# Optimization experiments

Measured on AMD Instinct MI355X. Metric: run time of the kernel, lower is better.

## Reference

```python
import jax, jax.numpy as jnp
import numpy as np

B, S, N, D = 2048, 8, 32, 64


def setup_inputs() -> dict:
    key = jax.random.key(0)
    ks = jax.random.split(key, 13)
    s1 = 1.0 / np.sqrt(2 * D + 6)
    s2 = 1.0 / np.sqrt(D)
    s3 = 1.0 / np.sqrt(D // 2)
    return {
        "celestial_tensor": jax.random.normal(ks[0], (B, S, N, D), jnp.float32),
        "theta": jax.random.normal(ks[1], (B, N), jnp.float32),
        "phi": jax.random.normal(ks[2], (B, N), jnp.float32),
        "velocity": jax.random.normal(ks[3], (B, N), jnp.float32),
        "radius": jax.random.uniform(ks[4], (B, N), jnp.float32),
        "longitude": jax.random.normal(ks[5], (B, N), jnp.float32),
        "W1": jax.random.uniform(ks[6], (2 * D + 6, D), jnp.float32, -s1, s1),
        "b1": jax.random.uniform(ks[7], (D,), jnp.float32, -s1, s1),
        "W2": jax.random.uniform(ks[8], (D, D // 2), jnp.float32, -s2, s2),
        "b2": jax.random.uniform(ks[9], (D // 2,), jnp.float32, -s2, s2),
        "W3": jax.random.uniform(ks[10], (D // 2, 1), jnp.float32, -s3, s3),
        "b3": jax.random.uniform(ks[11], (1,), jnp.float32, -s3, s3),
        "phase_weights": jnp.ones((6,), jnp.float32),
    }


def _circ(a, b):
    # circular difference wrapped to (-pi, pi]
    d = a - b
    return jnp.arctan2(jnp.sin(d), jnp.cos(d))


def reference(celestial_tensor, theta, phi, velocity, radius, longitude,
              W1, b1, W2, b2, W3, b3, phase_weights):
    Bb, _, Nn, _ = celestial_tensor.shape
    feats = celestial_tensor[:, -1]  # [B, N, D] last timestep
    ii, jj = np.triu_indices(Nn, 1)  # static upper-tri pair indices, P pairs
    fi = feats[:, ii]  # [B, P, D]
    fj = feats[:, jj]
    td = _circ(theta[:, ii], theta[:, jj])
    pd = _circ(phi[:, ii], phi[:, jj])
    vd = velocity[:, ii] - velocity[:, jj]
    rr = radius[:, ii] / (radius[:, jj] + 1e-8)
    ld = _circ(longitude[:, ii], longitude[:, jj])
    pr = jnp.cos(td) * jnp.cos(pd)  # phase_relationship
    scal = jnp.stack([td, pd, vd, rr, ld, pr], axis=-1)  # [B, P, 6]
    x = jnp.concatenate([fi, fj, scal], axis=-1)  # [B, P, 2D+6]
    h = jax.nn.gelu(x @ W1 + b1, approximate=False)
    h = jax.nn.gelu(h @ W2 + b2, approximate=False)
    edge = jax.nn.sigmoid((h @ W3 + b3)[..., 0])  # [B, P]
    pf = jnp.stack([jnp.abs(td), jnp.abs(pd), jnp.abs(vd),
                    jnp.abs(rr - 1.0), jnp.abs(ld), jnp.abs(pr)], axis=-1)
    gate = jax.nn.sigmoid(jnp.sum(pf * phase_weights, axis=-1))
    fe = edge * gate  # [B, P]
    adj = jnp.zeros((Bb, Nn, Nn), dtype=fe.dtype)
    adj = adj.at[:, ii, jj].set(fe).at[:, jj, ii].set(fe)
    return adj
```

## Files before the change

### kernel.cpp

```cpp
#include <hip/hip_runtime.h>
#include <hip/hip_bf16.h>
#include <math.h>

#define SS 8
#define NN 32
#define DD 64
#define NP 496
#define LDA 68

typedef short v8s __attribute__((ext_vector_type(8)));
typedef float v4f __attribute__((ext_vector_type(4)));
typedef float f2  __attribute__((ext_vector_type(2)));

union FragU { uint4 u; v8s s; };
union Q2    { float4 q; f2 h[2]; };

static __device__ __forceinline__ f2 f2m(float a, float b) { f2 r; r.x = a; r.y = b; return r; }
static __device__ __forceinline__ f2 splat2(float s) { f2 r; r.x = s; r.y = s; return r; }
static __device__ __forceinline__ f2 pk_fma(f2 a, f2 b, f2 c) {
#if __has_builtin(__builtin_elementwise_fma)
    return __builtin_elementwise_fma(a, b, c);
#else
    return f2m(fmaf(a.x, b.x, c.x), fmaf(a.y, b.y, c.y));
#endif
}

__device__ __forceinline__ float wrap_pi(float d) {
    return fmaf(-6.28318530717958647692f, rintf(d * 0.15915494309189533577f), d);
}
__device__ __forceinline__ float sigmoid_(float x) {
    return __builtin_amdgcn_rcpf(1.0f + __expf(-x));
}
__device__ __forceinline__ f2 gelu2(f2 x) {
#if __has_builtin(__builtin_elementwise_max)
    f2 ax = __builtin_elementwise_max(x, -x);
#else
    f2 ax = f2m(fabsf(x.x), fabsf(x.y));
#endif
    f2 az = ax * splat2(0.70710678118654752440f);
    f2 d = pk_fma(splat2(0.078108f), az, splat2(0.000972f));
    d = pk_fma(d, az, splat2(0.230389f));
    d = pk_fma(d, az, splat2(0.278393f));
    d = pk_fma(d, az, splat2(1.0f));
    f2 t = f2m(__builtin_amdgcn_rcpf(d.x), __builtin_amdgcn_rcpf(d.y));
    f2 t2 = t * t;
    f2 a = ax * splat2(0.5f);
    f2 base = pk_fma(x, splat2(0.5f), a);
    f2 u = a * t2;
    return pk_fma(-u, t2, base);
}
__device__ __forceinline__ unsigned int pack_bf16_rne(float x0, float x1) {
    union { __hip_bfloat162 h2; unsigned int u; } cv;
    float2 f; f.x = x0; f.y = x1;
    cv.h2 = __float22bfloat162_rn(f);
    return cv.u;
}
__device__ __forceinline__ float row_reduce16(float x) {
    int v;
    v = __builtin_amdgcn_update_dpp(0, __float_as_int(x), 0x128, 0xf, 0xf, false);
    x += __int_as_float(v);
    v = __builtin_amdgcn_update_dpp(0, __float_as_int(x), 0x124, 0xf, 0xf, false);
    x += __int_as_float(v);
    v = __builtin_amdgcn_update_dpp(0, __float_as_int(x), 0x122, 0xf, 0xf, false);
    x += __int_as_float(v);
    v = __builtin_amdgcn_update_dpp(0, __float_as_int(x), 0x121, 0xf, 0xf, false);
    x += __int_as_float(v);
    return x;
}
__device__ __forceinline__ uint4 build_w2_frag(const float* __restrict__ W2,
                                               int kb, int col) {
    uint4 pk;
    pk.x = pack_bf16_rne(W2[(kb + 0) * 32 + col], W2[(kb + 1) * 32 + col]);
    pk.y = pack_bf16_rne(W2[(kb + 2) * 32 + col], W2[(kb + 3) * 32 + col]);
    pk.z = pack_bf16_rne(W2[(kb + 4) * 32 + col], W2[(kb + 5) * 32 + col]);
    pk.w = pack_bf16_rne(W2[(kb + 6) * 32 + col], W2[(kb + 7) * 32 + col]);
    return pk;
}

__global__ __launch_bounds__(256, 2) void edge_kernel(
    const float* __restrict__ cel,
    const float* __restrict__ theta,
    const float* __restrict__ phi,
    const float* __restrict__ vel,
    const float* __restrict__ rad,
    const float* __restrict__ lon,
    const float* __restrict__ W1,
    const float* __restrict__ b1,
    const float* __restrict__ W2,
    const float* __restrict__ b2,
    const float* __restrict__ W3,
    const float* __restrict__ b3,
    const float* __restrict__ pw,
    float* __restrict__ out)
{
    __shared__ __align__(16) float sAi[NN * LDA];
    __shared__ __align__(16) float sBj[NN * LDA];
    __shared__ __align__(16) float sW1s[6 * 64];
    __shared__ float sAdj[1024];
    __shared__ __align__(16) float sScal[NP * 8];
    __shared__ unsigned char sI[NP], sJ[NP];

    const int b = blockIdx.x;
    const int t = threadIdx.x;
    const int ml = t & 15;
    const int ql = (t >> 4) & 3;
    const int wv = t >> 6;
    const int kA = ql * 8;

    FragU f00, f01, f10, f11;
    f00.u = build_w2_frag(W2, 0 * 32 + kA, 0 * 16 + ml);
    f01.u = build_w2_frag(W2, 1 * 32 + kA, 0 * 16 + ml);
    f10.u = build_w2_frag(W2, 0 * 32 + kA, 1 * 16 + ml);
    f11.u = build_w2_frag(W2, 1 * 32 + kA, 1 * 16 + ml);
    const float b2v0 = b2[ml], b2v1 = b2[16 + ml];
    const float w3v0 = W3[ml], w3v1 = W3[16 + ml];
    const float b3s  = b3[0];

    if (t < 31) {
        int off = t * 31 - (t * (t - 1)) / 2;
        for (int j = t + 1; j < 32; ++j) {
            sI[off] = (unsigned char)t;
            sJ[off] = (unsigned char)j;
            ++off;
        }
    }
    for (int idx = t; idx < 1024; idx += 256) sAdj[idx] = 0.0f;
    for (int idx = t; idx < 384; idx += 256) sW1s[idx] = W1[128 * 64 + idx];
    __syncthreads();

    for (int p = t; p < NP; p += 256) {
        const int i = sI[p], j = sJ[p];
        const float td = wrap_pi(theta[b * NN + i] - theta[b * NN + j]);
        const float pd = wrap_pi(phi[b * NN + i] - phi[b * NN + j]);
        const float vd = vel[b * NN + i] - vel[b * NN + j];
        const float rr = rad[b * NN + i] * __builtin_amdgcn_rcpf(rad[b * NN + j] + 1e-8f);
        const float ld = wrap_pi(lon[b * NN + i] - lon[b * NN + j]);
        const float pr = __cosf(td) * __cosf(pd);
        const float pf = fabsf(td) * pw[0] + fabsf(pd) * pw[1]
                       + fabsf(vd) * pw[2] + fabsf(rr - 1.0f) * pw[3]
                       + fabsf(ld) * pw[4] + fabsf(pr) * pw[5];
        const int sw = (p >> 2) & 1;
        float4* c0 = (float4*)&sScal[p * 8 + (sw << 2)];
        float4* c1 = (float4*)&sScal[p * 8 + ((sw ^ 1) << 2)];
        *c0 = float4{td, pd, vd, rr};
        *c1 = float4{ld, pr, sigmoid_(pf), 0.0f};
    }

    {
        const int col = t & 63;
        const int w   = __builtin_amdgcn_readfirstlane(t >> 6);
        const float* fbase = cel + ((size_t)b * SS + (SS - 1)) * (NN * DD);
        f2 accA[8], accB[8];
        #pragma unroll
        for (int m = 0; m < 8; ++m) { accA[m] = splat2(0.0f); accB[m] = splat2(0.0f); }
        for (int k4 = 0; k4 < 64; k4 += 4) {
            const f2 wa01 = f2m(W1[(k4 + 0) * 64 + col], W1[(k4 + 1) * 64 + col]);
            const f2 wa23 = f2m(W1[(k4 + 2) * 64 + col], W1[(k4 + 3) * 64 + col]);
            const f2 wb01 = f2m(W1[(k4 + 64) * 64 + col], W1[(k4 + 65) * 64 + col]);
            const f2 wb23 = f2m(W1[(k4 + 66) * 64 + col], W1[(k4 + 67) * 64 + col]);
            #pragma unroll
            for (int m = 0; m < 8; ++m) {
                const float4 fv = *(const float4*)&fbase[(w + 4 * m) * 64 + k4];
                accA[m] = pk_fma(f2m(fv.x, fv.y), wa01, accA[m]);
                accA[m] = pk_fma(f2m(fv.z, fv.w), wa23, accA[m]);
                accB[m] = pk_fma(f2m(fv.x, fv.y), wb01, accB[m]);
                accB[m] = pk_fma(f2m(fv.z, fv.w), wb23, accB[m]);
            }
        }
        const float b1c = b1[col];
        #pragma unroll
        for (int m = 0; m < 8; ++m) {
            sAi[(w + 4 * m) * LDA + col] = accA[m].x + accA[m].y + b1c;
            sBj[(w + 4 * m) * LDA + col] = accB[m].x + accB[m].y;
        }
    }
    __syncthreads();

    f2 w1f[6][8];
    #pragma unroll
    for (int s = 0; s < 6; ++s) {
        Q2 u0, u1, u2, u3;
        u0.q = *(const float4*)&sW1s[s * 64 + kA];
        u1.q = *(const float4*)&sW1s[s * 64 + kA + 4];
        u2.q = *(const float4*)&sW1s[s * 64 + 32 + kA];
        u3.q = *(const float4*)&sW1s[s * 64 + 36 + kA];
        w1f[s][0] = u0.h[0]; w1f[s][1] = u0.h[1];
        w1f[s][2] = u1.h[0]; w1f[s][3] = u1.h[1];
        w1f[s][4] = u2.h[0]; w1f[s][5] = u2.h[1];
        w1f[s][6] = u3.h[0]; w1f[s][7] = u3.h[1];
    }

    #pragma clang loop unroll(disable)
    for (int r = 0; r < 8; ++r) {
        const int mtl = r * 4 + wv;
        if (mtl >= 31) break;
        const int p = mtl * 16 + ml;
        const int i = sI[p], j = sJ[p];
        const int sw = (p >> 2) & 1;
        Q2 S0, S1;
        S0.q = *(const float4*)&sScal[p * 8 + (sw << 2)];
        S1.q = *(const float4*)&sScal[p * 8 + ((sw ^ 1) << 2)];
        const float sc[6] = {S0.q.x, S0.q.y, S0.q.z, S0.q.w, S1.q.x, S1.q.y};
        const float* Ar = &sAi[i * LDA];
        const float* Br = &sBj[j * LDA];

        FragU fa0, fa1;
        {
            Q2 P0, P1, Q0, Q1;
            P0.q = *(const float4*)(Ar + kA);
            P1.q = *(const float4*)(Ar + kA + 4);
            Q0.q = *(const float4*)(Br + kA);
            Q1.q = *(const float4*)(Br + kA + 4);
            f2 v[4] = {P0.h[0] + Q0.h[0], P0.h[1] + Q0.h[1],
                       P1.h[0] + Q1.h[0], P1.h[1] + Q1.h[1]};
            #pragma unroll
            for (int s = 0; s < 6; ++s) {
                const f2 scs = splat2(sc[s]);
                #pragma unroll
                for (int c = 0; c < 4; ++c)
                    v[c] = pk_fma(scs, w1f[s][c], v[c]);
            }
            #pragma unroll
            for (int c = 0; c < 4; ++c) v[c] = gelu2(v[c]);
            fa0.u.x = pack_bf16_rne(v[0].x, v[0].y);
            fa0.u.y = pack_bf16_rne(v[1].x, v[1].y);
            fa0.u.z = pack_bf16_rne(v[2].x, v[2].y);
            fa0.u.w = pack_bf16_rne(v[3].x, v[3].y);
        }
        {
            Q2 P2, P3, Q2v, Q3;
            P2.q  = *(const float4*)(Ar + 32 + kA);
            P3.q  = *(const float4*)(Ar + 36 + kA);
            Q2v.q = *(const float4*)(Br + 32 + kA);
            Q3.q  = *(const float4*)(Br + 36 + kA);
            f2 y[4] = {P2.h[0] + Q2v.h[0], P2.h[1] + Q2v.h[1],
                       P3.h[0] + Q3.h[0],  P3.h[1] + Q3.h[1]};
            #pragma unroll
            for (int s = 0; s < 6; ++s) {
                const f2 scs = splat2(sc[s]);
                #pragma unroll
                for (int c = 0; c < 4; ++c)
                    y[c] = pk_fma(scs, w1f[s][4 + c], y[c]);
            }
            #pragma unroll
            for (int c = 0; c < 4; ++c) y[c] = gelu2(y[c]);
            fa1.u.x = pack_bf16_rne(y[0].x, y[0].y);
            fa1.u.y = pack_bf16_rne(y[1].x, y[1].y);
            fa1.u.z = pack_bf16_rne(y[2].x, y[2].y);
            fa1.u.w = pack_bf16_rne(y[3].x, y[3].y);
        }

        v4f acc0 = {b2v0, b2v0, b2v0, b2v0};
        v4f acc1 = {b2v1, b2v1, b2v1, b2v1};
        acc0 = __builtin_amdgcn_mfma_f32_16x16x32_bf16(fa0.s, f00.s, acc0, 0, 0, 0);
        acc0 = __builtin_amdgcn_mfma_f32_16x16x32_bf16(fa1.s, f01.s, acc0, 0, 0, 0);
        acc1 = __builtin_amdgcn_mfma_f32_16x16x32_bf16(fa0.s, f10.s, acc1, 0, 0, 0);
        acc1 = __builtin_amdgcn_mfma_f32_16x16x32_bf16(fa1.s, f11.s, acc1, 0, 0, 0);

        float cres[4];
        #pragma unroll
        for (int rr = 0; rr < 4; ++rr) {
            const f2 g = gelu2(f2m(acc0[rr], acc1[rr]));
            cres[rr] = row_reduce16(fmaf(g.y, w3v1, g.x * w3v0));
        }
        const int rsel = ml & 3;
        const float cs = (rsel & 2) ? ((rsel & 1) ? cres[3] : cres[2])
                                    : ((rsel & 1) ? cres[1] : cres[0]);
        const int pe = mtl * 16 + ql * 4 + rsel;
        const int swe = (pe >> 2) & 1;
        const float gate = sScal[pe * 8 + ((swe ^ 1) << 2) + 2];
        const float fe = sigmoid_(cs + b3s) * gate;
        if (ml < 4) {
            const int pi = sI[pe], pj = sJ[pe];
            sAdj[pi * 32 + pj] = fe;
            sAdj[pj * 32 + pi] = fe;
        }
    }
    __syncthreads();

    float* dst = out + (size_t)b * 1024;
    for (int idx = t; idx < 1024; idx += 256) dst[idx] = sAdj[idx];
}

extern "C" void kernel_launch(void* const* d_in, const int* in_sizes, int n_in,
                              void* d_out, int out_size, void* d_ws, size_t ws_size,
                              hipStream_t stream) {
    const float* cel   = (const float*)d_in[0];
    const float* theta = (const float*)d_in[1];
    const float* phi   = (const float*)d_in[2];
    const float* vel   = (const float*)d_in[3];
    const float* rad   = (const float*)d_in[4];
    const float* lon   = (const float*)d_in[5];
    const float* W1    = (const float*)d_in[6];
    const float* b1    = (const float*)d_in[7];
    const float* W2    = (const float*)d_in[8];
    const float* b2    = (const float*)d_in[9];
    const float* W3    = (const float*)d_in[10];
    const float* b3    = (const float*)d_in[11];
    const float* pw    = (const float*)d_in[12];
    float* out = (float*)d_out;

    const int B = in_sizes[1] / NN;
    edge_kernel<<<B, 256, 0, stream>>>(cel, theta, phi, vel, rad, lon,
                                       W1, b1, W2, b2, W3, b3, pw, out);
}
```

Before: 256.8 us.

## Software-pipeline LDS operand loads across tiles and pack pair indices into one short

The per-wave tile loop now processes two tiles per iteration. The scalar features and the first half of the pair feature rows for the next tile are loaded from LDS while the current tile's FMA, GELU and MFMA work runs, so LDS latency is hidden behind compute. The i/j pair indices are packed into a single 16-bit shared array, so one LDS read replaces two. This raises register pressure under launch_bounds(256,2), which could cause spills or limit occupancy.

```diff
diff --git a/kernel.cpp b/kernel.cpp
--- a/kernel.cpp
+++ b/kernel.cpp
@@ -76,6 +76,91 @@
     pk.w = pack_bf16_rne(W2[(kb + 6) * 32 + col], W2[(kb + 7) * 32 + col]);
     return pk;
 }
+
+#define LOAD_IJ(DST, MTL) DST = sIJ[(MTL) * 16 + ml];
+#define LOAD_RS(S0v, S1v, P0v, P1v, Q0v, Q1v, IJv, MTL)                    \
+    {                                                                       \
+        const int lp_ = (MTL) * 16 + ml;                                    \
+        const int lsw_ = (lp_ >> 2) & 1;                                    \
+        S0v.q = *(const float4*)&sScal[lp_ * 8 + (lsw_ << 2)];              \
+        S1v.q = *(const float4*)&sScal[lp_ * 8 + ((lsw_ ^ 1) << 2)];        \
+        const int li_ = (IJv) & 255, lj_ = (IJv) >> 8;                      \
+        P0v.q = *(const float4*)&sAi[li_ * LDA + kA];                       \
+        P1v.q = *(const float4*)&sAi[li_ * LDA + kA + 4];                   \
+        Q0v.q = *(const float4*)&sBj[lj_ * LDA + kA];                       \
+        Q1v.q = *(const float4*)&sBj[lj_ * LDA + kA + 4];                   \
+    }
+#define COMPUTE_TILE(S0v, S1v, P0v, P1v, Q0v, Q1v, IJv, MTL)               \
+    {                                                                       \
+        const int ci_ = (IJv) & 255, cj_ = (IJv) >> 8;                      \
+        Q2 P2_, P3_, R2_, R3_;                                              \
+        P2_.q = *(const float4*)&sAi[ci_ * LDA + 32 + kA];                  \
+        P3_.q = *(const float4*)&sAi[ci_ * LDA + 36 + kA];                  \
+        R2_.q = *(const float4*)&sBj[cj_ * LDA + 32 + kA];                  \
+        R3_.q = *(const float4*)&sBj[cj_ * LDA + 36 + kA];                  \
+        const float sc_[6] = {S0v.q.x, S0v.q.y, S0v.q.z, S0v.q.w,           \
+                              S1v.q.x, S1v.q.y};                            \
+        FragU fa0_, fa1_;                                                   \
+        {                                                                   \
+            f2 v_[4] = {P0v.h[0] + Q0v.h[0], P0v.h[1] + Q0v.h[1],           \
+                        P1v.h[0] + Q1v.h[0], P1v.h[1] + Q1v.h[1]};          \
+            _Pragma("unroll")                                               \
+            for (int s_ = 0; s_ < 6; ++s_) {                                \
+                const f2 scs_ = splat2(sc_[s_]);                            \
+                _Pragma("unroll")                                           \
+                for (int c_ = 0; c_ < 4; ++c_)                              \
+                    v_[c_] = pk_fma(scs_, w1f[s_][c_], v_[c_]);             \
+            }                                                               \
+            _Pragma("unroll")                                               \
+            for (int c_ = 0; c_ < 4; ++c_) v_[c_] = gelu2(v_[c_]);          \
+            fa0_.u.x = pack_bf16_rne(v_[0].x, v_[0].y);                     \
+            fa0_.u.y = pack_bf16_rne(v_[1].x, v_[1].y);                     \
+            fa0_.u.z = pack_bf16_rne(v_[2].x, v_[2].y);                     \
+            fa0_.u.w = pack_bf16_rne(v_[3].x, v_[3].y);                     \
+        }                                                                   \
+        {                                                                   \
+            f2 y_[4] = {P2_.h[0] + R2_.h[0], P2_.h[1] + R2_.h[1],           \
+                        P3_.h[0] + R3_.h[0], P3_.h[1] + R3_.h[1]};          \
+            _Pragma("unroll")                                               \
+            for (int s_ = 0; s_ < 6; ++s_) {                                \
+                const f2 scs_ = splat2(sc_[s_]);                            \
+                _Pragma("unroll")                                           \
+                for (int c_ = 0; c_ < 4; ++c_)                              \
+                    y_[c_] = pk_fma(scs_, w1f[s_][4 + c_], y_[c_]);         \
+            }                                                               \
+            _Pragma("unroll")                                               \
+            for (int c_ = 0; c_ < 4; ++c_) y_[c_] = gelu2(y_[c_]);          \
+            fa1_.u.x = pack_bf16_rne(y_[0].x, y_[0].y);                     \
+            fa1_.u.y = pack_bf16_rne(y_[1].x, y_[1].y);                     \
+            fa1_.u.z = pack_bf16_rne(y_[2].x, y_[2].y);                     \
+            fa1_.u.w = pack_bf16_rne(y_[3].x, y_[3].y);                     \
+        }                                                                   \
+        v4f acc0_ = {b2v0, b2v0, b2v0, b2v0};                               \
+        v4f acc1_ = {b2v1, b2v1, b2v1, b2v1};                               \
+        acc0_ = __builtin_amdgcn_mfma_f32_16x16x32_bf16(fa0_.s, f00.s, acc0_, 0, 0, 0); \
+        acc0_ = __builtin_amdgcn_mfma_f32_16x16x32_bf16(fa1_.s, f01.s, acc0_, 0, 0, 0); \
+        acc1_ = __builtin_amdgcn_mfma_f32_16x16x32_bf16(fa0_.s, f10.s, acc1_, 0, 0, 0); \
+        acc1_ = __builtin_amdgcn_mfma_f32_16x16x32_bf16(fa1_.s, f11.s, acc1_, 0, 0, 0); \
+        float cres_[4];                                                     \
+        _Pragma("unroll")                                                   \
+        for (int q_ = 0; q_ < 4; ++q_) {                                    \
+            const f2 g_ = gelu2(f2m(acc0_[q_], acc1_[q_]));                 \
+            cres_[q_] = row_reduce16(fmaf(g_.y, w3v1, g_.x * w3v0));        \
+        }                                                                   \
+        const int rsel_ = ml & 3;                                           \
+        const float cs_ = (rsel_ & 2) ? ((rsel_ & 1) ? cres_[3] : cres_[2]) \
+                                      : ((rsel_ & 1) ? cres_[1] : cres_[0]);\
+        const int pe_ = (MTL) * 16 + ql * 4 + rsel_;                        \
+        const int swe_ = (pe_ >> 2) & 1;                                    \
+        const float gate_ = sScal[pe_ * 8 + ((swe_ ^ 1) << 2) + 2];         \
+        const float fe_ = sigmoid_(cs_ + b3s) * gate_;                      \
+        if (ml < 4) {                                                       \
+            const int ije_ = sIJ[pe_];                                      \
+            const int pi_ = ije_ & 255, pj_ = ije_ >> 8;                    \
+            sAdj[pi_ * 32 + pj_] = fe_;                                     \
+            sAdj[pj_ * 32 + pi_] = fe_;                                     \
+        }                                                                   \
+    }
 
 __global__ __launch_bounds__(256, 2) void edge_kernel(
     const float* __restrict__ cel,
@@ -98,7 +183,7 @@
     __shared__ __align__(16) float sW1s[6 * 64];
     __shared__ float sAdj[1024];
     __shared__ __align__(16) float sScal[NP * 8];
-    __shared__ unsigned char sI[NP], sJ[NP];
+    __shared__ unsigned short sIJ[NP];
 
     const int b = blockIdx.x;
     const int t = threadIdx.x;
@@ -119,8 +204,7 @@
     if (t < 31) {
         int off = t * 31 - (t * (t - 1)) / 2;
         for (int j = t + 1; j < 32; ++j) {
-            sI[off] = (unsigned char)t;
-            sJ[off] = (unsigned char)j;
+            sIJ[off] = (unsigned short)(t | (j << 8));
             ++off;
         }
     }
@@ -129,7 +213,8 @@
     __syncthreads();
 
     for (int p = t; p < NP; p += 256) {
-        const int i = sI[p], j = sJ[p];
+        const int ij = sIJ[p];
+        const int i = ij & 255, j = ij >> 8;
         const float td = wrap_pi(theta[b * NN + i] - theta[b * NN + j]);
         const float pd = wrap_pi(phi[b * NN + i] - phi[b * NN + j]);
         const float vd = vel[b * NN + i] - vel[b * NN + j];
@@ -190,91 +275,31 @@
         w1f[s][6] = u3.h[0]; w1f[s][7] = u3.h[1];
     }
 
+    int ijA, ijB;
+    Q2 SA0, SA1, PA0, PA1, QA0, QA1;
+    Q2 SB0, SB1, PB0, PB1, QB0, QB1;
+    LOAD_IJ(ijA, wv);
+    LOAD_RS(SA0, SA1, PA0, PA1, QA0, QA1, ijA, wv);
+    LOAD_IJ(ijB, 4 + wv);
+
     #pragma clang loop unroll(disable)
-    for (int r = 0; r < 8; ++r) {
-        const int mtl = r * 4 + wv;
-        if (mtl >= 31) break;
-        const int p = mtl * 16 + ml;
-        const int i = sI[p], j = sJ[p];
-        const int sw = (p >> 2) & 1;
-        Q2 S0, S1;
-        S0.q = *(const float4*)&sScal[p * 8 + (sw << 2)];
-        S1.q = *(const float4*)&sScal[p * 8 + ((sw ^ 1) << 2)];
-        const float sc[6] = {S0.q.x, S0.q.y, S0.q.z, S0.q.w, S1.q.x, S1.q.y};
-        const float* Ar = &sAi[i * LDA];
-        const float* Br = &sBj[j * LDA];
-
-        FragU fa0, fa1;
-        {
-            Q2 P0, P1, Q0, Q1;
-            P0.q = *(const float4*)(Ar + kA);
-            P1.q = *(const float4*)(Ar + kA + 4);
-            Q0.q = *(const float4*)(Br + kA);
-            Q1.q = *(const float4*)(Br + kA + 4);
-            f2 v[4] = {P0.h[0] + Q0.h[0], P0.h[1] + Q0.h[1],
-                       P1.h[0] + Q1.h[0], P1.h[1] + Q1.h[1]};
-            #pragma unroll
-            for (int s = 0; s < 6; ++s) {
-                const f2 scs = splat2(sc[s]);
-                #pragma unroll
-                for (int c = 0; c < 4; ++c)
-                    v[c] = pk_fma(scs, w1f[s][c], v[c]);
-            }
-            #pragma unroll
-            for (int c = 0; c < 4; ++c) v[c] = gelu2(v[c]);
-            fa0.u.x = pack_bf16_rne(v[0].x, v[0].y);
-            fa0.u.y = pack_bf16_rne(v[1].x, v[1].y);
-            fa0.u.z = pack_bf16_rne(v[2].x, v[2].y);
-            fa0.u.w = pack_bf16_rne(v[3].x, v[3].y);
-        }
-        {
-            Q2 P2, P3, Q2v, Q3;
-            P2.q  = *(const float4*)(Ar + 32 + kA);
-            P3.q  = *(const float4*)(Ar + 36 + kA);
-            Q2v.q = *(const float4*)(Br + 32 + kA);
-            Q3.q  = *(const float4*)(Br + 36 + kA);
-            f2 y[4] = {P2.h[0] + Q2v.h[0], P2.h[1] + Q2v.h[1],
-                       P3.h[0] + Q3.h[0],  P3.h[1] + Q3.h[1]};
-            #pragma unroll
-            for (int s = 0; s < 6; ++s) {
-                const f2 scs = splat2(sc[s]);
-                #pragma unroll
-                for (int c = 0; c < 4; ++c)
-                    y[c] = pk_fma(scs, w1f[s][4 + c], y[c]);
-            }
-            #pragma unroll
-            for (int c = 0; c < 4; ++c) y[c] = gelu2(y[c]);
-            fa1.u.x = pack_bf16_rne(y[0].x, y[0].y);
-            fa1.u.y = pack_bf16_rne(y[1].x, y[1].y);
-            fa1.u.z = pack_bf16_rne(y[2].x, y[2].y);
-            fa1.u.w = pack_bf16_rne(y[3].x, y[3].y);
-        }
-
-        v4f acc0 = {b2v0, b2v0, b2v0, b2v0};
-        v4f acc1 = {b2v1, b2v1, b2v1, b2v1};
-        acc0 = __builtin_amdgcn_mfma_f32_16x16x32_bf16(fa0.s, f00.s, acc0, 0, 0, 0);
-        acc0 = __builtin_amdgcn_mfma_f32_16x16x32_bf16(fa1.s, f01.s, acc0, 0, 0, 0);
-        acc1 = __builtin_amdgcn_mfma_f32_16x16x32_bf16(fa0.s, f10.s, acc1, 0, 0, 0);
-        acc1 = __builtin_amdgcn_mfma_f32_16x16x32_bf16(fa1.s, f11.s, acc1, 0, 0, 0);
-
-        float cres[4];
-        #pragma unroll
-        for (int rr = 0; rr < 4; ++rr) {
-            const f2 g = gelu2(f2m(acc0[rr], acc1[rr]));
-            cres[rr] = row_reduce16(fmaf(g.y, w3v1, g.x * w3v0));
-        }
-        const int rsel = ml & 3;
-        const float cs = (rsel & 2) ? ((rsel & 1) ? cres[3] : cres[2])
-                                    : ((rsel & 1) ? cres[1] : cres[0]);
-        const int pe = mtl * 16 + ql * 4 + rsel;
-        const int swe = (pe >> 2) & 1;
-        const float gate = sScal[pe * 8 + ((swe ^ 1) << 2) + 2];
-        const float fe = sigmoid_(cs + b3s) * gate;
-        if (ml < 4) {
-            const int pi = sI[pe], pj = sJ[pe];
-            sAdj[pi * 32 + pj] = fe;
-            sAdj[pj * 32 + pi] = fe;
-        }
+    for (int rr = 0; rr < 4; ++rr) {
+        const int mtl0 = rr * 8 + wv;
+        const int mtl1 = mtl0 + 4;
+        const bool v1 = (mtl1 < 31);
+        const int mtl1c = v1 ? mtl1 : 30;
+        const int mtl2c = (mtl0 + 8 < 31) ? (mtl0 + 8) : 30;
+        const int mtl3c = (mtl1 + 8 < 31) ? (mtl1 + 8) : 30;
+
+        LOAD_RS(SB0, SB1, PB0, PB1, QB0, QB1, ijB, mtl1c);
+        const int ij0_ = ijA;
+        LOAD_IJ(ijA, mtl2c);
+        COMPUTE_TILE(SA0, SA1, PA0, PA1, QA0, QA1, ij0_, mtl0);
+
+        LOAD_RS(SA0, SA1, PA0, PA1, QA0, QA1, ijA, mtl2c);
+        const int ij1_ = ijB;
+        LOAD_IJ(ijB, mtl3c);
+        if (v1) COMPUTE_TILE(SB0, SB1, PB0, PB1, QB0, QB1, ij1_, mtl1);
     }
     __syncthreads();
 
```

New measurement: 265.5 us. 1.03x slower.
